# Performance work log

Hardware: AMD Instinct MI355X
Metric: run time of the kernel (lower is better)

Reference implementation:

```python
import jax, jax.numpy as jnp
import numpy as np

N_NODES = 100000
N_EDGES = 1600000
H, D, DE = 4, 32, 32  # heads, node_out_feats, edge_out_feats
NEG_SLOPE = 0.2


def setup_inputs() -> dict:
    key = jax.random.key(0)
    ks = jax.random.split(key, 10)
    return {
        "node_inputs": jax.random.normal(ks[0], (N_NODES, 128), jnp.float32),
        "edge_inputs": jax.random.normal(ks[1], (N_EDGES, 16), jnp.float32),
        "src": jax.random.randint(ks[2], (N_EDGES,), 0, N_NODES, jnp.int32),
        "dst": jax.random.randint(ks[3], (N_EDGES,), 0, N_NODES, jnp.int32),
        "W_fc": jax.random.normal(ks[4], (128, H * D), jnp.float32) * 0.1,
        "attn_src_p": jax.random.normal(ks[5], (1, H, D), jnp.float32) * 0.1,
        "attn_dst_p": jax.random.normal(ks[6], (1, H, D), jnp.float32) * 0.1,
        "W_edge": jax.random.normal(ks[7], (16, H * DE), jnp.float32) * 0.1,
        "attn_edge_p": jax.random.normal(ks[8], (1, H, DE), jnp.float32) * 0.1,
        "W_res": jax.random.normal(ks[9], (128, H * D), jnp.float32) * 0.1,
        "bias_p": jnp.zeros((H * D,), jnp.float32),
    }


def reference(node_inputs, edge_inputs, src, dst, W_fc, attn_src_p,
              attn_dst_p, W_edge, attn_edge_p, W_res, bias_p):
    N = node_inputs.shape[0]
    # node projection: [N, H, D]
    feat = (node_inputs @ W_fc).reshape(N, H, D)
    # per-node attention logits [N, H]
    a_src = (feat * attn_src_p).sum(-1)
    a_dst = (feat * attn_dst_p).sum(-1)
    # edge-feature attention logits [E, H]
    feat_e = (edge_inputs @ W_edge).reshape(-1, H, DE)
    a_edge = (feat_e * attn_edge_p).sum(-1)
    # per-edge score: u_add_v + edge term, then LeakyReLU
    e = a_src[src] + a_dst[dst] + a_edge                 # [E, H]
    e = jnp.where(e > 0, e, NEG_SLOPE * e)
    # edge softmax grouped by destination node
    emax = jax.lax.stop_gradient(jax.ops.segment_max(e, dst, num_segments=N))
    ex = jnp.exp(e - emax[dst])
    denom = jax.ops.segment_sum(ex, dst, num_segments=N)
    attn = ex / denom[dst]                               # [E, H]
    # weighted scatter-aggregate of source features
    msg = feat[src] * attn[:, :, None]                   # [E, H, D]
    x = jax.ops.segment_sum(msg, dst, num_segments=N)    # [N, H, D]
    # residual + bias
    x = x + (node_inputs @ W_res).reshape(N, H, D)
    x = x + bias_p.reshape(H, D)
    return x
```

## Files before the change

### kernel.cpp

```cpp
#include <hip/hip_runtime.h>
#include <math.h>

#define NNODES_FEAT 128
#define HD 128
#define H 4
#define D 32
#define EDGE_F 16
#define NEG_SLOPE 0.2f

typedef _Float16 f16;
typedef _Float16 f16x2 __attribute__((ext_vector_type(2)));
typedef _Float16 f16x4 __attribute__((ext_vector_type(4)));
typedef _Float16 f16x8 __attribute__((ext_vector_type(8)));
typedef float f32x4 __attribute__((ext_vector_type(4)));

union ExPack { float2 f; f16x4 h; };

__global__ void k_wedge(const float* __restrict__ W_edge,
                        const float* __restrict__ attn_edge,
                        float* __restrict__ w_eh) {
    int t = threadIdx.x;
    int k = t >> 2;
    int h = t & 3;
    float s = 0.f;
    for (int d = 0; d < D; ++d)
        s += W_edge[k * HD + h * D + d] * attn_edge[h * D + d];
    w_eh[k * H + h] = s;
}

__global__ __launch_bounds__(256) void k_wt(const float* __restrict__ Wfc,
                                            const float* __restrict__ Wres,
                                            f16* __restrict__ Wt) {
    int i = blockIdx.x * 256 + threadIdx.x;
    int n = i >> 7, k = i & 127;
    float v = (n < 128) ? Wfc[k * HD + n] : Wres[k * HD + (n - 128)];
    Wt[(size_t)n * 128 + k] = (f16)v;
}

#define LDK 136
__global__ __launch_bounds__(256) void k_gemm_mfma(
    const float* __restrict__ A, const f16* __restrict__ Wt,
    const float* __restrict__ bias, const float* __restrict__ asp,
    const float* __restrict__ adp, f16* __restrict__ feat16,
    float* __restrict__ a_src, float* __restrict__ a_dst,
    float* __restrict__ out, int N) {
    __shared__ f16 As[64 * LDK];
    __shared__ f16 Bs[128 * LDK];
    int tid = threadIdx.x;
    int wave = tid >> 6, lane = tid & 63;
    int m0 = blockIdx.x * 64;

    for (int c = tid; c < 64 * 32; c += 256) {
        int r = c >> 5, cc = (c & 31) * 4;
        int gr = m0 + r;
        float4 v = make_float4(0.f, 0.f, 0.f, 0.f);
        if (gr < N) v = *(const float4*)(A + (size_t)gr * 128 + cc);
        f16x4 h = {(f16)v.x, (f16)v.y, (f16)v.z, (f16)v.w};
        *(f16x4*)(&As[r * LDK + cc]) = h;
    }

    int am = lane & 15, aq = lane >> 4;
    int arow = wave * 16 + am;
    int orow0 = m0 + wave * 16 + aq * 4;

    for (int cb = 0; cb < 2; ++cb) {
        if (cb) __syncthreads();
        const f16* Wblk = Wt + (size_t)cb * 128 * 128;
        for (int c = tid; c < 128 * 16; c += 256) {
            int r = c >> 4, cc = (c & 15) * 8;
            float4 v = *(const float4*)(Wblk + (size_t)r * 128 + cc);
            *(float4*)(&Bs[r * LDK + cc]) = v;
        }
        __syncthreads();

        f32x4 acc[8];
#pragma unroll
        for (int nt = 0; nt < 8; ++nt) acc[nt] = (f32x4){0.f, 0.f, 0.f, 0.f};
#pragma unroll
        for (int kc = 0; kc < 4; ++kc) {
            f16x8 a = *(const f16x8*)(&As[arow * LDK + kc * 32 + aq * 8]);
#pragma unroll
            for (int nt = 0; nt < 8; ++nt) {
                f16x8 b = *(const f16x8*)(&Bs[(nt * 16 + am) * LDK + kc * 32 + aq * 8]);
                acc[nt] = __builtin_amdgcn_mfma_f32_16x16x32_f16(a, b, acc[nt], 0, 0, 0);
            }
        }

        if (cb == 0) {
#pragma unroll
            for (int nt = 0; nt < 8; ++nt) {
                int col = nt * 16 + am;
#pragma unroll
                for (int r = 0; r < 4; ++r) {
                    int row = orow0 + r;
                    if (row < N) feat16[(size_t)row * 128 + col] = (f16)acc[nt][r];
                }
            }
            float w1v[8], w2v[8];
#pragma unroll
            for (int nt = 0; nt < 8; ++nt) {
                w1v[nt] = asp[nt * 16 + am];
                w2v[nt] = adp[nt * 16 + am];
            }
#pragma unroll
            for (int r = 0; r < 4; ++r) {
                float p1[4] = {0.f, 0.f, 0.f, 0.f};
                float p2[4] = {0.f, 0.f, 0.f, 0.f};
#pragma unroll
                for (int nt = 0; nt < 8; ++nt) {
                    int h = nt >> 1;
                    p1[h] += acc[nt][r] * w1v[nt];
                    p2[h] += acc[nt][r] * w2v[nt];
                }
#pragma unroll
                for (int off = 1; off < 16; off <<= 1) {
#pragma unroll
                    for (int h = 0; h < 4; ++h) {
                        p1[h] += __shfl_xor(p1[h], off);
                        p2[h] += __shfl_xor(p2[h], off);
                    }
                }
                int row = orow0 + r;
                if (row < N) {
                    if (am < 4) {
                        float v = am == 0 ? p1[0] : am == 1 ? p1[1] : am == 2 ? p1[2] : p1[3];
                        a_src[row * 4 + am] = v;
                    } else if (am < 8) {
                        int hh = am - 4;
                        float v = hh == 0 ? p2[0] : hh == 1 ? p2[1] : hh == 2 ? p2[2] : p2[3];
                        a_dst[row * 4 + hh] = v;
                    }
                }
            }
        } else {
#pragma unroll
            for (int nt = 0; nt < 8; ++nt) {
                int col = nt * 16 + am;
                float bv = bias[col];
#pragma unroll
                for (int r = 0; r < 4; ++r) {
                    int row = orow0 + r;
                    if (row < N) out[(size_t)row * 128 + col] = acc[nt][r] + bv;
                }
            }
        }
    }
}

__global__ __launch_bounds__(256) void k_edge_logit(
    const float* __restrict__ edge_inputs, const int* __restrict__ src,
    const int* __restrict__ dst, const float* __restrict__ w_eh,
    const float* __restrict__ a_src, const float* __restrict__ a_dst,
    int* __restrict__ deg, int* __restrict__ rank,
    float2* __restrict__ evp, int E) {
    __shared__ float weh_s[EDGE_F * H];
    if (threadIdx.x < EDGE_F * H) weh_s[threadIdx.x] = w_eh[threadIdx.x];
    __syncthreads();

    int base = blockIdx.x * 512 + threadIdx.x;
    int e0 = base, e1 = base + 256;
    bool v0 = e0 < E, v1 = e1 < E;

    int s0 = v0 ? src[e0] : 0, s1 = v1 ? src[e1] : 0;
    int d0 = v0 ? dst[e0] : 0, d1 = v1 ? dst[e1] : 0;

    float4 xa[4], xb[4];
    if (v0) {
        const float* x = edge_inputs + (size_t)e0 * EDGE_F;
        xa[0] = *(const float4*)(x);      xa[1] = *(const float4*)(x + 4);
        xa[2] = *(const float4*)(x + 8);  xa[3] = *(const float4*)(x + 12);
    }
    if (v1) {
        const float* x = edge_inputs + (size_t)e1 * EDGE_F;
        xb[0] = *(const float4*)(x);      xb[1] = *(const float4*)(x + 4);
        xb[2] = *(const float4*)(x + 8);  xb[3] = *(const float4*)(x + 12);
    }

    float4 as0 = *(const float4*)(a_src + s0 * H);
    float4 ad0 = *(const float4*)(a_dst + d0 * H);
    float4 as1 = *(const float4*)(a_src + s1 * H);
    float4 ad1 = *(const float4*)(a_dst + d1 * H);

    int r0 = v0 ? atomicAdd(deg + d0, 1) : 0;
    int r1 = v1 ? atomicAdd(deg + d1, 1) : 0;

    if (v0) {
        float ae0 = 0.f, ae1 = 0.f, ae2 = 0.f, ae3 = 0.f;
        const float* xs = (const float*)xa;
#pragma unroll
        for (int k = 0; k < EDGE_F; ++k) {
            float xv = xs[k];
            ae0 += xv * weh_s[k * H + 0];
            ae1 += xv * weh_s[k * H + 1];
            ae2 += xv * weh_s[k * H + 2];
            ae3 += xv * weh_s[k * H + 3];
        }
        float ev[H];
        ev[0] = as0.x + ad0.x + ae0;
        ev[1] = as0.y + ad0.y + ae1;
        ev[2] = as0.z + ad0.z + ae2;
        ev[3] = as0.w + ad0.w + ae3;
#pragma unroll
        for (int h = 0; h < H; ++h) {
            float t = ev[h];
            t = t > 0.f ? t : NEG_SLOPE * t;
            ev[h] = __expf(t);
        }
        ExPack p;
        p.h = (f16x4){(f16)ev[0], (f16)ev[1], (f16)ev[2], (f16)ev[3]};
        evp[e0] = p.f;
        rank[e0] = r0;
    }
    if (v1) {
        float ae0 = 0.f, ae1 = 0.f, ae2 = 0.f, ae3 = 0.f;
        const float* xs = (const float*)xb;
#pragma unroll
        for (int k = 0; k < EDGE_F; ++k) {
            float xv = xs[k];
            ae0 += xv * weh_s[k * H + 0];
            ae1 += xv * weh_s[k * H + 1];
            ae2 += xv * weh_s[k * H + 2];
            ae3 += xv * weh_s[k * H + 3];
        }
        float ev[H];
        ev[0] = as1.x + ad1.x + ae0;
        ev[1] = as1.y + ad1.y + ae1;
        ev[2] = as1.z + ad1.z + ae2;
        ev[3] = as1.w + ad1.w + ae3;
#pragma unroll
        for (int h = 0; h < H; ++h) {
            float t = ev[h];
            t = t > 0.f ? t : NEG_SLOPE * t;
            ev[h] = __expf(t);
        }
        ExPack p;
        p.h = (f16x4){(f16)ev[0], (f16)ev[1], (f16)ev[2], (f16)ev[3]};
        evp[e1] = p.f;
        rank[e1] = r1;
    }
}

__global__ __launch_bounds__(256) void k_scan_partial(
    const int* __restrict__ deg, int* __restrict__ partial, int N) {
    __shared__ int sdata[256];
    int t = threadIdx.x;
    int base = blockIdx.x * 1024 + t * 4;
    int s = 0;
#pragma unroll
    for (int j = 0; j < 4; ++j) { int i = base + j; if (i < N) s += deg[i]; }
    sdata[t] = s;
    __syncthreads();
    for (int off = 128; off > 0; off >>= 1) {
        if (t < off) sdata[t] += sdata[t + off];
        __syncthreads();
    }
    if (t == 0) partial[blockIdx.x] = sdata[0];
}

__global__ __launch_bounds__(256) void k_scan_top(
    int* __restrict__ partial, int* __restrict__ offs, int nb, int N) {
    __shared__ int sdata[256];
    int t = threadIdx.x;
    int v = (t < nb) ? partial[t] : 0;
    sdata[t] = v;
    __syncthreads();
    for (int off = 1; off < 256; off <<= 1) {
        int add = (t >= off) ? sdata[t - off] : 0;
        __syncthreads();
        sdata[t] += add;
        __syncthreads();
    }
    int excl = (t == 0) ? 0 : sdata[t - 1];
    if (t < nb) partial[t] = excl;
    if (t == nb - 1) offs[N] = sdata[t];
}

__global__ __launch_bounds__(256) void k_scan_final(
    int* __restrict__ deg_offs, const int* __restrict__ partial, int N) {
    __shared__ int sdata[256];
    int t = threadIdx.x;
    int base = blockIdx.x * 1024 + t * 4;
    int v[4]; int s = 0;
#pragma unroll
    for (int j = 0; j < 4; ++j) { int i = base + j; v[j] = (i < N) ? deg_offs[i] : 0; s += v[j]; }
    sdata[t] = s;
    __syncthreads();
    for (int off = 1; off < 256; off <<= 1) {
        int add = (t >= off) ? sdata[t - off] : 0;
        __syncthreads();
        sdata[t] += add;
        __syncthreads();
    }
    int excl = partial[blockIdx.x] + ((t == 0) ? 0 : sdata[t - 1]);
#pragma unroll
    for (int j = 0; j < 4; ++j) {
        int i = base + j;
        if (i < N) { deg_offs[i] = excl; excl += v[j]; }
    }
}

__global__ __launch_bounds__(256) void k_permute(
    const int* __restrict__ src, const int* __restrict__ dst,
    const int* __restrict__ rank, const float2* __restrict__ evp,
    const int* __restrict__ offs, float4* __restrict__ rec, int E) {
    int base = blockIdx.x * 1024 + threadIdx.x;
    int s[4], d[4], r[4]; float2 q[4]; bool v[4];
#pragma unroll
    for (int j = 0; j < 4; ++j) {
        int e = base + j * 256;
        v[j] = e < E;
        s[j] = v[j] ? src[e] : 0;
        d[j] = v[j] ? dst[e] : 0;
        r[j] = v[j] ? rank[e] : 0;
        q[j] = v[j] ? evp[e] : make_float2(0.f, 0.f);
    }
    int pos[4];
#pragma unroll
    for (int j = 0; j < 4; ++j) pos[j] = offs[d[j]] + r[j];
#pragma unroll
    for (int j = 0; j < 4; ++j) {
        if (!v[j]) continue;
        float4 rr;
        rr.x = __int_as_float(s[j]);
        rr.y = q[j].x;
        rr.z = q[j].y;
        rr.w = 0.f;
        rec[pos[j]] = rr;
    }
}

__device__ __forceinline__ float exsel(float a, float b, int hword, int hshift) {
    unsigned u = __float_as_uint(hword ? b : a);
    unsigned short us = (unsigned short)(u >> hshift);
    f16 hv;
    __builtin_memcpy(&hv, &us, 2);
    return (float)hv;
}

__global__ __launch_bounds__(256) void k_aggr(
    const f16* __restrict__ feat16, const float4* __restrict__ rec,
    const int* __restrict__ offs, float* __restrict__ out, int N) {
    int wave = threadIdx.x >> 6;
    int lane = threadIdx.x & 63;
    int n = blockIdx.x * 4 + wave;
    if (n >= N) return;
    int beg = offs[n], end = offs[n + 1];
    if (end <= beg) return;
    int hword = (lane >> 5) & 1;
    int hshift = ((lane >> 4) & 1) * 16;
    size_t c0 = (size_t)2 * lane;
    float num0 = 0.f, num1 = 0.f, den = 0.f;
    int i = beg;
    for (; i + 3 < end; i += 4) {
        float4 r0 = rec[i], r1 = rec[i + 1], r2 = rec[i + 2], r3 = rec[i + 3];
        int s0 = __float_as_int(r0.x), s1 = __float_as_int(r1.x);
        int s2 = __float_as_int(r2.x), s3 = __float_as_int(r3.x);
        f16x2 f0 = *(const f16x2*)(feat16 + (size_t)s0 * HD + c0);
        f16x2 f1 = *(const f16x2*)(feat16 + (size_t)s1 * HD + c0);
        f16x2 f2 = *(const f16x2*)(feat16 + (size_t)s2 * HD + c0);
        f16x2 f3 = *(const f16x2*)(feat16 + (size_t)s3 * HD + c0);
        float e0 = exsel(r0.y, r0.z, hword, hshift);
        float e1 = exsel(r1.y, r1.z, hword, hshift);
        float e2 = exsel(r2.y, r2.z, hword, hshift);
        float e3 = exsel(r3.y, r3.z, hword, hshift);
        num0 += e0 * (float)f0.x + e1 * (float)f1.x + e2 * (float)f2.x + e3 * (float)f3.x;
        num1 += e0 * (float)f0.y + e1 * (float)f1.y + e2 * (float)f2.y + e3 * (float)f3.y;
        den += e0 + e1 + e2 + e3;
    }
    for (; i < end; ++i) {
        float4 r0 = rec[i];
        int s0 = __float_as_int(r0.x);
        f16x2 f0 = *(const f16x2*)(feat16 + (size_t)s0 * HD + c0);
        float e0 = exsel(r0.y, r0.z, hword, hshift);
        num0 += e0 * (float)f0.x;
        num1 += e0 * (float)f0.y;
        den += e0;
    }
    float inv = 1.f / den;
    size_t o = (size_t)n * HD + c0;
    float2 v = *(float2*)(out + o);
    v.x += num0 * inv;
    v.y += num1 * inv;
    *(float2*)(out + o) = v;
}

extern "C" void kernel_launch(void* const* d_in, const int* in_sizes, int n_in,
                              void* d_out, int out_size, void* d_ws, size_t ws_size,
                              hipStream_t stream) {
    const float* node_inputs = (const float*)d_in[0];
    const float* edge_inputs = (const float*)d_in[1];
    const int*   src         = (const int*)d_in[2];
    const int*   dst         = (const int*)d_in[3];
    const float* W_fc        = (const float*)d_in[4];
    const float* attn_src_p  = (const float*)d_in[5];
    const float* attn_dst_p  = (const float*)d_in[6];
    const float* W_edge      = (const float*)d_in[7];
    const float* attn_edge_p = (const float*)d_in[8];
    const float* W_res       = (const float*)d_in[9];
    const float* bias_p      = (const float*)d_in[10];

    int N = in_sizes[0] / NNODES_FEAT;
    int E = in_sizes[2];

    float* out = (float*)d_out;

    f16*    feat16  = (f16*)d_ws;
    float4* rec     = (float4*)(feat16 + (size_t)N * HD);
    f16*    Wt      = (f16*)(rec + (size_t)E);
    float*  a_src   = (float*)(Wt + 256 * 128);
    float*  a_dst   = a_src + (size_t)N * H;
    float*  w_eh    = a_dst + (size_t)N * H;
    int*    deg     = (int*)(w_eh + 64);
    int*    offs    = deg;
    int*    partial = deg + (N + 2);
    int*    rank    = partial + 128;
    float2* evp     = (float2*)(rank + (size_t)E);

    hipMemsetAsync(deg, 0, (size_t)(N + 2) * sizeof(int), stream);

    k_wedge<<<1, 64, 0, stream>>>(W_edge, attn_edge_p, w_eh);
    k_wt<<<(256 * 128) / 256, 256, 0, stream>>>(W_fc, W_res, Wt);

    int gb = (N + 63) / 64;
    k_gemm_mfma<<<gb, 256, 0, stream>>>(node_inputs, Wt, bias_p, attn_src_p,
                                        attn_dst_p, feat16, a_src, a_dst, out, N);

    int eb = (E + 511) / 512;
    k_edge_logit<<<eb, 256, 0, stream>>>(edge_inputs, src, dst, w_eh, a_src, a_dst,
                                         deg, rank, evp, E);

    int sb = (N + 1023) / 1024;
    k_scan_partial<<<sb, 256, 0, stream>>>(deg, partial, N);
    k_scan_top<<<1, 256, 0, stream>>>(partial, offs, sb, N);
    k_scan_final<<<sb, 256, 0, stream>>>(deg, partial, N);

    int pb = (E + 1023) / 1024;
    k_permute<<<pb, 256, 0, stream>>>(src, dst, rank, evp, offs, rec, E);

    int ab = (N + 3) / 4;
    k_aggr<<<ab, 256, 0, stream>>>(feat16, rec, offs, out, N);
}
```

Before: 446.4 us.

## Batch edge-logit work per thread, vectorize scans, use fdot2 in aggregation

The edge-logit kernel now handles four edges per thread and issues all index loads, atomics and gathers before the compute, which exposes more memory-level parallelism. The scan kernels use int4 vector loads and stores on full chunks. The aggregation kernel packs f16 weights and features with perm and accumulates with packed fdot2 instructions and 32-bit address arithmetic, cutting conversion and ALU work. Accumulating through fdot2 changes rounding slightly and raises register use per thread.

```diff
diff --git a/kernel.cpp b/kernel.cpp
--- a/kernel.cpp
+++ b/kernel.cpp
@@ -157,36 +157,37 @@
     if (threadIdx.x < EDGE_F * H) weh_s[threadIdx.x] = w_eh[threadIdx.x];
     __syncthreads();
 
-    int base = blockIdx.x * 512 + threadIdx.x;
-    int e0 = base, e1 = base + 256;
-    bool v0 = e0 < E, v1 = e1 < E;
-
-    int s0 = v0 ? src[e0] : 0, s1 = v1 ? src[e1] : 0;
-    int d0 = v0 ? dst[e0] : 0, d1 = v1 ? dst[e1] : 0;
-
-    float4 xa[4], xb[4];
-    if (v0) {
-        const float* x = edge_inputs + (size_t)e0 * EDGE_F;
-        xa[0] = *(const float4*)(x);      xa[1] = *(const float4*)(x + 4);
-        xa[2] = *(const float4*)(x + 8);  xa[3] = *(const float4*)(x + 12);
-    }
-    if (v1) {
-        const float* x = edge_inputs + (size_t)e1 * EDGE_F;
-        xb[0] = *(const float4*)(x);      xb[1] = *(const float4*)(x + 4);
-        xb[2] = *(const float4*)(x + 8);  xb[3] = *(const float4*)(x + 12);
-    }
-
-    float4 as0 = *(const float4*)(a_src + s0 * H);
-    float4 ad0 = *(const float4*)(a_dst + d0 * H);
-    float4 as1 = *(const float4*)(a_src + s1 * H);
-    float4 ad1 = *(const float4*)(a_dst + d1 * H);
-
-    int r0 = v0 ? atomicAdd(deg + d0, 1) : 0;
-    int r1 = v1 ? atomicAdd(deg + d1, 1) : 0;
-
-    if (v0) {
+    int base = blockIdx.x * 1024 + threadIdx.x;
+    int e[4], s[4], d[4]; bool v[4];
+#pragma unroll
+    for (int j = 0; j < 4; ++j) {
+        e[j] = base + j * 256;
+        v[j] = e[j] < E;
+        s[j] = v[j] ? src[e[j]] : 0;
+        d[j] = v[j] ? dst[e[j]] : 0;
+    }
+    int rk[4];
+#pragma unroll
+    for (int j = 0; j < 4; ++j) rk[j] = v[j] ? atomicAdd(deg + d[j], 1) : 0;
+
+    float4 as[4], ad[4];
+#pragma unroll
+    for (int j = 0; j < 4; ++j) {
+        as[j] = *(const float4*)(a_src + (unsigned)s[j] * 4u);
+        ad[j] = *(const float4*)(a_dst + (unsigned)d[j] * 4u);
+    }
+
+#pragma unroll
+    for (int j = 0; j < 4; ++j) {
+        if (!v[j]) continue;
+        const float* x = edge_inputs + (size_t)e[j] * EDGE_F;
+        float4 x0 = *(const float4*)(x);
+        float4 x1 = *(const float4*)(x + 4);
+        float4 x2 = *(const float4*)(x + 8);
+        float4 x3 = *(const float4*)(x + 12);
+        float xs[16] = {x0.x, x0.y, x0.z, x0.w, x1.x, x1.y, x1.z, x1.w,
+                        x2.x, x2.y, x2.z, x2.w, x3.x, x3.y, x3.z, x3.w};
         float ae0 = 0.f, ae1 = 0.f, ae2 = 0.f, ae3 = 0.f;
-        const float* xs = (const float*)xa;
 #pragma unroll
         for (int k = 0; k < EDGE_F; ++k) {
             float xv = xs[k];
@@ -196,10 +197,10 @@
             ae3 += xv * weh_s[k * H + 3];
         }
         float ev[H];
-        ev[0] = as0.x + ad0.x + ae0;
-        ev[1] = as0.y + ad0.y + ae1;
-        ev[2] = as0.z + ad0.z + ae2;
-        ev[3] = as0.w + ad0.w + ae3;
+        ev[0] = as[j].x + ad[j].x + ae0;
+        ev[1] = as[j].y + ad[j].y + ae1;
+        ev[2] = as[j].z + ad[j].z + ae2;
+        ev[3] = as[j].w + ad[j].w + ae3;
 #pragma unroll
         for (int h = 0; h < H; ++h) {
             float t = ev[h];
@@ -208,35 +209,8 @@
         }
         ExPack p;
         p.h = (f16x4){(f16)ev[0], (f16)ev[1], (f16)ev[2], (f16)ev[3]};
-        evp[e0] = p.f;
-        rank[e0] = r0;
-    }
-    if (v1) {
-        float ae0 = 0.f, ae1 = 0.f, ae2 = 0.f, ae3 = 0.f;
-        const float* xs = (const float*)xb;
-#pragma unroll
-        for (int k = 0; k < EDGE_F; ++k) {
-            float xv = xs[k];
-            ae0 += xv * weh_s[k * H + 0];
-            ae1 += xv * weh_s[k * H + 1];
-            ae2 += xv * weh_s[k * H + 2];
-            ae3 += xv * weh_s[k * H + 3];
-        }
-        float ev[H];
-        ev[0] = as1.x + ad1.x + ae0;
-        ev[1] = as1.y + ad1.y + ae1;
-        ev[2] = as1.z + ad1.z + ae2;
-        ev[3] = as1.w + ad1.w + ae3;
-#pragma unroll
-        for (int h = 0; h < H; ++h) {
-            float t = ev[h];
-            t = t > 0.f ? t : NEG_SLOPE * t;
-            ev[h] = __expf(t);
-        }
-        ExPack p;
-        p.h = (f16x4){(f16)ev[0], (f16)ev[1], (f16)ev[2], (f16)ev[3]};
-        evp[e1] = p.f;
-        rank[e1] = r1;
+        evp[e[j]] = p.f;
+        rank[e[j]] = rk[j];
     }
 }
 
@@ -246,8 +220,13 @@
     int t = threadIdx.x;
     int base = blockIdx.x * 1024 + t * 4;
     int s = 0;
-#pragma unroll
-    for (int j = 0; j < 4; ++j) { int i = base + j; if (i < N) s += deg[i]; }
+    if (base + 3 < N) {
+        int4 v4 = *(const int4*)(deg + base);
+        s = v4.x + v4.y + v4.z + v4.w;
+    } else {
+#pragma unroll
+        for (int j = 0; j < 4; ++j) { int i = base + j; if (i < N) s += deg[i]; }
+    }
     sdata[t] = s;
     __syncthreads();
     for (int off = 128; off > 0; off >>= 1) {
@@ -281,8 +260,14 @@
     int t = threadIdx.x;
     int base = blockIdx.x * 1024 + t * 4;
     int v[4]; int s = 0;
-#pragma unroll
-    for (int j = 0; j < 4; ++j) { int i = base + j; v[j] = (i < N) ? deg_offs[i] : 0; s += v[j]; }
+    if (base + 3 < N) {
+        int4 v4 = *(const int4*)(deg_offs + base);
+        v[0] = v4.x; v[1] = v4.y; v[2] = v4.z; v[3] = v4.w;
+        s = v[0] + v[1] + v[2] + v[3];
+    } else {
+#pragma unroll
+        for (int j = 0; j < 4; ++j) { int i = base + j; v[j] = (i < N) ? deg_offs[i] : 0; s += v[j]; }
+    }
     sdata[t] = s;
     __syncthreads();
     for (int off = 1; off < 256; off <<= 1) {
@@ -292,10 +277,19 @@
         __syncthreads();
     }
     int excl = partial[blockIdx.x] + ((t == 0) ? 0 : sdata[t - 1]);
-#pragma unroll
-    for (int j = 0; j < 4; ++j) {
-        int i = base + j;
-        if (i < N) { deg_offs[i] = excl; excl += v[j]; }
+    if (base + 3 < N) {
+        int4 w;
+        w.x = excl;
+        w.y = excl + v[0];
+        w.z = excl + v[0] + v[1];
+        w.w = excl + v[0] + v[1] + v[2];
+        *(int4*)(deg_offs + base) = w;
+    } else {
+#pragma unroll
+        for (int j = 0; j < 4; ++j) {
+            int i = base + j;
+            if (i < N) { deg_offs[i] = excl; excl += v[j]; }
+        }
     }
 }
 
@@ -329,12 +323,20 @@
     }
 }
 
-__device__ __forceinline__ float exsel(float a, float b, int hword, int hshift) {
+__device__ __forceinline__ unsigned ex16(float a, float b, int hword, int hshift) {
     unsigned u = __float_as_uint(hword ? b : a);
-    unsigned short us = (unsigned short)(u >> hshift);
-    f16 hv;
-    __builtin_memcpy(&hv, &us, 2);
-    return (float)hv;
+    return (u >> hshift) & 0xffffu;
+}
+__device__ __forceinline__ f16x2 u2h(unsigned u) {
+    f16x2 h; __builtin_memcpy(&h, &u, 4); return h;
+}
+__device__ __forceinline__ float fdot2f(unsigned a, unsigned b, float c) {
+#if defined(__has_builtin) && __has_builtin(__builtin_amdgcn_fdot2)
+    return __builtin_amdgcn_fdot2(u2h(a), u2h(b), c, false);
+#else
+    f16x2 ha = u2h(a), hb = u2h(b);
+    return c + (float)ha[0] * (float)hb[0] + (float)ha[1] * (float)hb[1];
+#endif
 }
 
 __global__ __launch_bounds__(256) void k_aggr(
@@ -348,32 +350,36 @@
     if (end <= beg) return;
     int hword = (lane >> 5) & 1;
     int hshift = ((lane >> 4) & 1) * 16;
-    size_t c0 = (size_t)2 * lane;
+    unsigned c0 = (unsigned)(lane << 1);
+    const unsigned uones = 0x3C003C00u;
     float num0 = 0.f, num1 = 0.f, den = 0.f;
     int i = beg;
     for (; i + 3 < end; i += 4) {
         float4 r0 = rec[i], r1 = rec[i + 1], r2 = rec[i + 2], r3 = rec[i + 3];
-        int s0 = __float_as_int(r0.x), s1 = __float_as_int(r1.x);
-        int s2 = __float_as_int(r2.x), s3 = __float_as_int(r3.x);
-        f16x2 f0 = *(const f16x2*)(feat16 + (size_t)s0 * HD + c0);
-        f16x2 f1 = *(const f16x2*)(feat16 + (size_t)s1 * HD + c0);
-        f16x2 f2 = *(const f16x2*)(feat16 + (size_t)s2 * HD + c0);
-        f16x2 f3 = *(const f16x2*)(feat16 + (size_t)s3 * HD + c0);
-        float e0 = exsel(r0.y, r0.z, hword, hshift);
-        float e1 = exsel(r1.y, r1.z, hword, hshift);
-        float e2 = exsel(r2.y, r2.z, hword, hshift);
-        float e3 = exsel(r3.y, r3.z, hword, hshift);
-        num0 += e0 * (float)f0.x + e1 * (float)f1.x + e2 * (float)f2.x + e3 * (float)f3.x;
-        num1 += e0 * (float)f0.y + e1 * (float)f1.y + e2 * (float)f2.y + e3 * (float)f3.y;
-        den += e0 + e1 + e2 + e3;
+        unsigned f0 = *(const unsigned*)(feat16 + (((unsigned)__float_as_int(r0.x) << 7) | c0));
+        unsigned f1 = *(const unsigned*)(feat16 + (((unsigned)__float_as_int(r1.x) << 7) | c0));
+        unsigned f2 = *(const unsigned*)(feat16 + (((unsigned)__float_as_int(r2.x) << 7) | c0));
+        unsigned f3 = *(const unsigned*)(feat16 + (((unsigned)__float_as_int(r3.x) << 7) | c0));
+        unsigned e01 = ex16(r0.y, r0.z, hword, hshift) | (ex16(r1.y, r1.z, hword, hshift) << 16);
+        unsigned e23 = ex16(r2.y, r2.z, hword, hshift) | (ex16(r3.y, r3.z, hword, hshift) << 16);
+        unsigned x01 = __builtin_amdgcn_perm(f1, f0, 0x05040100u);
+        unsigned y01 = __builtin_amdgcn_perm(f1, f0, 0x07060302u);
+        unsigned x23 = __builtin_amdgcn_perm(f3, f2, 0x05040100u);
+        unsigned y23 = __builtin_amdgcn_perm(f3, f2, 0x07060302u);
+        num0 = fdot2f(e01, x01, num0);
+        num1 = fdot2f(e01, y01, num1);
+        num0 = fdot2f(e23, x23, num0);
+        num1 = fdot2f(e23, y23, num1);
+        den  = fdot2f(e01, uones, den);
+        den  = fdot2f(e23, uones, den);
     }
     for (; i < end; ++i) {
         float4 r0 = rec[i];
-        int s0 = __float_as_int(r0.x);
-        f16x2 f0 = *(const f16x2*)(feat16 + (size_t)s0 * HD + c0);
-        float e0 = exsel(r0.y, r0.z, hword, hshift);
-        num0 += e0 * (float)f0.x;
-        num1 += e0 * (float)f0.y;
+        unsigned f0 = *(const unsigned*)(feat16 + (((unsigned)__float_as_int(r0.x) << 7) | c0));
+        float e0 = (float)u2h(ex16(r0.y, r0.z, hword, hshift))[0];
+        f16x2 fh = u2h(f0);
+        num0 += e0 * (float)fh[0];
+        num1 += e0 * (float)fh[1];
         den += e0;
     }
     float inv = 1.f / den;
@@ -425,7 +431,7 @@
     k_gemm_mfma<<<gb, 256, 0, stream>>>(node_inputs, Wt, bias_p, attn_src_p,
                                         attn_dst_p, feat16, a_src, a_dst, out, N);
 
-    int eb = (E + 511) / 512;
+    int eb = (E + 1023) / 1024;
     k_edge_logit<<<eb, 256, 0, stream>>>(edge_inputs, src, dst, w_eh, a_src, a_dst,
                                          deg, rank, evp, E);
 
```

Result: slower. 480.6 us (+7.7%).
